# Optimization experiments

Hardware: AMD Instinct MI355X
Metric: run time of the kernel (lower is better)

The kernel has to match this reference:

```python
import jax, jax.numpy as jnp
import numpy as np

N = 50000      # nodes
E = 800000     # edges
F_IN = 256
HID = [256, 256, 512]
G = 512        # graphs
FP = 2048      # fingerprint size


def setup_inputs() -> dict:
    key = jax.random.key(0)
    ks = jax.random.split(key, 14)
    node_features = jax.random.normal(ks[0], (N, F_IN), dtype=jnp.float32)
    edge_index = jax.random.randint(ks[1], (2, E), 0, N, dtype=jnp.int64)
    batch = jnp.sort(jax.random.randint(ks[2], (N,), 0, G, dtype=jnp.int64))

    def lin(k, fi, fo):
        s = 1.0 / np.sqrt(fi)
        kw, kb = jax.random.split(k)
        W = jax.random.uniform(kw, (fi, fo), jnp.float32, -s, s)
        b = jax.random.uniform(kb, (fo,), jnp.float32, -s, s)
        return W, b

    W1, b1 = lin(ks[3], F_IN, HID[0])
    W2, b2 = lin(ks[4], HID[0], HID[1])
    W3, b3 = lin(ks[5], HID[1], HID[2])
    pw, pb = lin(ks[6], HID[2], 1)          # PoolWeightedSum gating linear
    Wo, bo = lin(ks[7], 2 * HID[2], FP)     # head: weight_sum + max concat
    return dict(node_features=node_features, edge_index=edge_index, batch=batch,
                W1=W1, b1=b1, W2=W2, b2=b2, W3=W3, b3=b3,
                pw=pw, pb=pb, Wo=Wo, bo=bo)


def _gcn_layer(x, src, dst, W, b):
    # GCNConv: add self-loops, symmetric normalization, h = x @ W, aggregate.
    n = x.shape[0]
    h = x @ W  # [N, F_out]
    loop = jnp.arange(n, dtype=src.dtype)
    s = jnp.concatenate([src, loop])
    d = jnp.concatenate([dst, loop])
    deg = jax.ops.segment_sum(jnp.ones(s.shape[0], h.dtype), d, num_segments=n)
    dis = jax.lax.rsqrt(deg)  # deg >= 1 because of self-loops
    norm = dis[s] * dis[d]    # [E+N]
    out = jax.ops.segment_sum(h[s] * norm[:, None], d, num_segments=n)
    return out + b


def _forward(node_features, edge_index, batch,
             W1, b1, W2, b2, W3, b3, pw, pb, Wo, bo):
    src, dst = edge_index[0], edge_index[1]
    x = node_features
    for W, b in ((W1, b1), (W2, b2), (W3, b3)):
        x = jax.nn.relu(_gcn_layer(x, src, dst, W, b))

    # PoolWeightedSum: sigmoid-gated node features, scatter-add per graph
    w = jax.nn.sigmoid(x @ pw + pb)  # [N, 1]
    pooled_ws = jax.ops.segment_sum(x * w, batch, num_segments=G,
                                    indices_are_sorted=True)
    # PoolMax: scatter-max per graph (empty segments -> 0, like torch zeros init)
    pooled_max = jax.ops.segment_max(x, batch, num_segments=G,
                                     indices_are_sorted=True)
    pooled_max = jnp.where(jnp.isfinite(pooled_max), pooled_max, 0.0)

    feats = jnp.concatenate([pooled_ws, pooled_max], axis=1)  # [G, 2*HID[-1]]
    return jax.nn.relu(feats @ Wo + bo)  # [G, FP]


def reference(node_features, edge_index, batch,
              W1, b1, W2, b2, W3, b3, pw, pb, Wo, bo):
    return _forward(node_features, edge_index, batch,
                    W1, b1, W2, b2, W3, b3, pw, pb, Wo, bo)
```

## Files before the change

### kernel.cpp

```cpp
#include <hip/hip_runtime.h>
#include <math.h>

#define NNODES 50000
#define NEDGES 800000
#define NGRAPH 512
#define FIN    256
#define H1     256
#define H2     256
#define H3     512
#define FPOUT  2048

typedef __attribute__((ext_vector_type(8))) short short8;
typedef __attribute__((ext_vector_type(8))) _Float16 half8;
typedef __attribute__((ext_vector_type(4))) float floatx4;
typedef __attribute__((ext_vector_type(4))) unsigned short ushx4;

__device__ inline float h2f(ushort u) { return (float)__builtin_bit_cast(_Float16, u); }
__device__ inline ushort f2h(float x) { return __builtin_bit_cast(ushort, (_Float16)x); }
__device__ inline void split2h(float a, ushort& h, ushort& l) {
    _Float16 hh = (_Float16)a;
    h = __builtin_bit_cast(ushort, hh);
    l = f2h(a - (float)hh);
}


__global__ __launch_bounds__(256) void zero_i32(int* p, int n) {
    int i = blockIdx.x * 256 + threadIdx.x;
    if (i < n) p[i] = 0;
}

__global__ __launch_bounds__(256) void count_deg(const int* __restrict__ ei, int* __restrict__ degi,
                                                 int* __restrict__ rank, int e_total) {
    int e = blockIdx.x * 256 + threadIdx.x;
    if (e >= e_total) return;
    int d = ei[e_total + e];
    rank[e] = atomicAdd(&degi[d], 1);
}

__global__ __launch_bounds__(256) void calc_dis(const int* __restrict__ degi, float* __restrict__ dis, int n) {
    int i = blockIdx.x * 256 + threadIdx.x;
    if (i < n) dis[i] = rsqrtf((float)(degi[i] + 1));
}

__global__ __launch_bounds__(256) void scanA(const int* __restrict__ degi, int* __restrict__ offs,
                                             int* __restrict__ partials, int n) {
    __shared__ int sm[256];
    int t = threadIdx.x, idx = blockIdx.x * 256 + t;
    int v = (idx < n) ? degi[idx] : 0;
    sm[t] = v; __syncthreads();
    for (int d = 1; d < 256; d <<= 1) {
        int add = (t >= d) ? sm[t - d] : 0;
        __syncthreads();
        sm[t] += add;
        __syncthreads();
    }
    if (idx < n) offs[idx + 1] = sm[t];
    if (t == 255) partials[blockIdx.x] = sm[255];
}

__global__ __launch_bounds__(256) void scanB(int* __restrict__ partials, int nb) {
    __shared__ int sm[256];
    int t = threadIdx.x;
    int v = (t < nb) ? partials[t] : 0;
    sm[t] = v; __syncthreads();
    for (int d = 1; d < 256; d <<= 1) {
        int add = (t >= d) ? sm[t - d] : 0;
        __syncthreads();
        sm[t] += add;
        __syncthreads();
    }
    if (t < nb) partials[t] = sm[t] - v;
}

__global__ __launch_bounds__(256) void scanC(int* __restrict__ offs, const int* __restrict__ partials, int n) {
    int idx = blockIdx.x * 256 + threadIdx.x;
    if (idx < n) offs[idx + 1] += partials[blockIdx.x];
    if (idx == 0) offs[0] = 0;
}

__global__ __launch_bounds__(256) void fill_csr(const int* __restrict__ ei, const float* __restrict__ dis,
                                                const int* __restrict__ offs, const int* __restrict__ rank,
                                                int2* __restrict__ csr_pair, int e_total) {
    int e = blockIdx.x * 256 + threadIdx.x;
    if (e >= e_total) return;
    int s = ei[e];
    int d = ei[e_total + e];
    int pos = offs[d] + rank[e];
    int2 pr;
    pr.x = s;
    pr.y = __float_as_int(dis[s] * dis[d]);
    csr_pair[pos] = pr;
}

__global__ __launch_bounds__(256) void wsplit_t(const float* __restrict__ W, ushort* __restrict__ hi,
                                                ushort* __restrict__ lo, int K, int N) {
    __shared__ float sm[32][33];
    int tx = threadIdx.x & 31, ty = threadIdx.x >> 5;
    int n0 = blockIdx.x * 32, k0 = blockIdx.y * 32;
    #pragma unroll
    for (int j = 0; j < 32; j += 8)
        sm[ty + j][tx] = W[(size_t)(k0 + ty + j) * N + n0 + tx];
    __syncthreads();
    #pragma unroll
    for (int j = 0; j < 32; j += 8) {
        float a = sm[tx][ty + j];
        ushort h, l; split2h(a, h, l);
        size_t o = (size_t)(n0 + ty + j) * K + k0 + tx;
        hi[o] = h; lo[o] = l;
    }
}

__global__ __launch_bounds__(256) void conv_f16(const float* __restrict__ x, ushort* __restrict__ xh, int total4) {
    int i = blockIdx.x * 256 + threadIdx.x;
    if (i >= total4) return;
    float4 a = ((const float4*)x)[i];
    ushx4 h = {f2h(a.x), f2h(a.y), f2h(a.z), f2h(a.w)};
    ((ushx4*)xh)[i] = h;
}

template<int SPLIT, int ACC, int KSPAN>
__global__ __launch_bounds__(256) void gemm_f16(const ushort* __restrict__ Ahp, const ushort* __restrict__ Alp,
                                                const ushort* __restrict__ Bhp, const ushort* __restrict__ Blp,
                                                float* __restrict__ C, ushort* __restrict__ Ch,
                                                const float* __restrict__ bias,
                                                int M, int N, int K, int do_relu, int outmode) {
    __shared__ _Float16 lsA[128 * 64];
    __shared__ _Float16 lsB[128 * 64];
    __shared__ _Float16 lsAl[SPLIT ? 128 * 64 : 8];
    __shared__ _Float16 lsBl[SPLIT ? 128 * 64 : 8];
    const _Float16* Ah = (const _Float16*)Ahp;
    const _Float16* Al = (const _Float16*)Alp;
    const _Float16* Bh = (const _Float16*)Bhp;
    const _Float16* Bl = (const _Float16*)Blp;

    int tid = threadIdx.x;
    int w = tid >> 6, lane = tid & 63;
    int quad = lane >> 4, lr = lane & 15;
    int wm = w & 1, wn = w >> 1;

    int gx = gridDim.x;
    int orig = blockIdx.y * gx + blockIdx.x;
    int nwg = gx * gridDim.y;
    int xcd = orig & 7, slot = orig >> 3;
    int q = nwg >> 3, r = nwg & 7;
    int wid = (xcd < r ? xcd * (q + 1) : r * (q + 1) + (xcd - r) * q) + slot;
    int row0 = (wid / gx) * 128, col0 = (wid % gx) * 128;
    int kb = blockIdx.z * KSPAN;

    floatx4 acc[4][4];
    #pragma unroll
    for (int i = 0; i < 4; ++i)
        #pragma unroll
        for (int j = 0; j < 4; ++j)
            acc[i][j] = (floatx4){0.f, 0.f, 0.f, 0.f};

    const half8 zer = {};
    int srow = tid >> 3;
    int sgran = tid & 7;
    int skk = sgran * 8;
    int sgx = (sgran ^ (srow & 7)) * 8;

    half8 pa[4], pb[4], pal[4], pbl[4];
    #pragma unroll
    for (int c = 0; c < 4; ++c) {
        int row = c * 32 + srow;
        bool mok = (row0 + row) < M;
        size_t aoff = (size_t)(row0 + row) * K + kb + skk;
        pa[c] = mok ? *(const half8*)(Ah + aoff) : zer;
        if constexpr (SPLIT) pal[c] = mok ? *(const half8*)(Al + aoff) : zer;
        size_t boff = (size_t)(col0 + row) * K + kb + skk;
        pb[c] = *(const half8*)(Bh + boff);
        if constexpr (SPLIT) pbl[c] = *(const half8*)(Bl + boff);
    }

    for (int k0 = kb; k0 < kb + KSPAN; k0 += 64) {
        #pragma unroll
        for (int c = 0; c < 4; ++c) {
            int lo = (c * 32 + srow) * 64 + sgx;
            *(half8*)(lsA + lo) = pa[c];
            *(half8*)(lsB + lo) = pb[c];
            if constexpr (SPLIT) { *(half8*)(lsAl + lo) = pal[c]; *(half8*)(lsBl + lo) = pbl[c]; }
        }
        __syncthreads();
        if (k0 + 64 < kb + KSPAN) {
            #pragma unroll
            for (int c = 0; c < 4; ++c) {
                int row = c * 32 + srow;
                bool mok = (row0 + row) < M;
                size_t aoff = (size_t)(row0 + row) * K + k0 + 64 + skk;
                pa[c] = mok ? *(const half8*)(Ah + aoff) : zer;
                if constexpr (SPLIT) pal[c] = mok ? *(const half8*)(Al + aoff) : zer;
                size_t boff = (size_t)(col0 + row) * K + k0 + 64 + skk;
                pb[c] = *(const half8*)(Bh + boff);
                if constexpr (SPLIT) pbl[c] = *(const half8*)(Bl + boff);
            }
        }
        #pragma unroll
        for (int kk = 0; kk < 2; ++kk) {
            half8 af[4], afl[4];
            #pragma unroll
            for (int mt = 0; mt < 4; ++mt) {
                int row = wm * 64 + mt * 16 + lr;
                int ao = row * 64 + (((kk * 4 + quad) ^ (row & 7)) << 3);
                af[mt] = *(const half8*)(lsA + ao);
                if constexpr (SPLIT) afl[mt] = *(const half8*)(lsAl + ao);
            }
            #pragma unroll
            for (int nt = 0; nt < 4; ++nt) {
                int row = wn * 64 + nt * 16 + lr;
                int bo = row * 64 + (((kk * 4 + quad) ^ (row & 7)) << 3);
                half8 bf = *(const half8*)(lsB + bo);
                half8 bfl;
                if constexpr (SPLIT) bfl = *(const half8*)(lsBl + bo);
                #pragma unroll
                for (int mt = 0; mt < 4; ++mt) {
                    acc[mt][nt] = __builtin_amdgcn_mfma_f32_16x16x32_f16(af[mt], bf, acc[mt][nt], 0, 0, 0);
                    if constexpr (SPLIT) {
                        acc[mt][nt] = __builtin_amdgcn_mfma_f32_16x16x32_f16(af[mt], bfl, acc[mt][nt], 0, 0, 0);
                        acc[mt][nt] = __builtin_amdgcn_mfma_f32_16x16x32_f16(afl[mt], bf, acc[mt][nt], 0, 0, 0);
                    }
                }
            }
        }
        __syncthreads();
    }

    size_t zoff = ACC ? (size_t)blockIdx.z * M * N : 0;
    #pragma unroll
    for (int mt = 0; mt < 4; ++mt) {
        #pragma unroll
        for (int rr = 0; rr < 4; ++rr) {
            int row = row0 + wm * 64 + mt * 16 + quad * 4 + rr;
            if (row >= M) continue;
            #pragma unroll
            for (int nt = 0; nt < 4; ++nt) {
                int col = col0 + wn * 64 + nt * 16 + lr;
                float v = acc[mt][nt][rr];
                if (!ACC) {
                    v += bias[col];
                    if (do_relu) v = v > 0.f ? v : 0.f;
                }
                if (outmode) Ch[(size_t)row * N + col] = f2h(v);
                else         C[zoff + (size_t)row * N + col] = v;
            }
        }
    }
}

__global__ __launch_bounds__(256) void head_fin(const float* __restrict__ part, const float* __restrict__ bo,
                                                float* __restrict__ out) {
    int i4 = blockIdx.x * 256 + threadIdx.x;
    const int TOT4 = NGRAPH * FPOUT / 4;
    if (i4 >= TOT4) return;
    int col4 = i4 & (FPOUT / 4 - 1);
    const size_t STRIDE4 = (size_t)NGRAPH * FPOUT / 4;
    const float4* p = (const float4*)part;
    float4 a = p[i4];
    float4 b = p[i4 + STRIDE4];
    float4 c = p[i4 + 2 * STRIDE4];
    float4 d = p[i4 + 3 * STRIDE4];
    float4 bb = ((const float4*)bo)[col4];
    float4 o;
    o.x = a.x + b.x + c.x + d.x + bb.x; o.x = o.x > 0.f ? o.x : 0.f;
    o.y = a.y + b.y + c.y + d.y + bb.y; o.y = o.y > 0.f ? o.y : 0.f;
    o.z = a.z + b.z + c.z + d.z + bb.z; o.z = o.z > 0.f ? o.z : 0.f;
    o.w = a.w + b.w + c.w + d.w + bb.w; o.w = o.w > 0.f ? o.w : 0.f;
    ((float4*)out)[i4] = o;
}

__global__ __launch_bounds__(256) void agg256b(const ushort* __restrict__ xh, ushort* __restrict__ yh,
                                               const float* __restrict__ dis,
                                               const int* __restrict__ offs, const int2* __restrict__ csr_pair) {
    constexpr int F = 256;
    int wave = threadIdx.x >> 6;
    int lane = threadIdx.x & 63;
    int half = lane >> 5;
    int sub  = lane & 31;
    int v = blockIdx.x * 8 + wave * 2 + half;
    int beg = offs[v], end = offs[v + 1];
    int len = end - beg;
    int leno = __shfl_xor(len, 32, 64);
    int maxlen = len > leno ? len : leno;

    float dv = dis[v];
    float sw = dv * dv;
    short8 a0 = ((const short8*)(xh + (size_t)v * F))[sub];
    float acc[8];
    #pragma unroll
    for (int j = 0; j < 8; ++j) acc[j] = h2f((ushort)a0[j]) * sw;

    for (int k = 0; k < maxlen; k += 8) {
        int   s[8];
        float w[8];
        #pragma unroll
        for (int u = 0; u < 8; ++u) {
            int idx = beg + k + u;
            bool val = idx < end;
            int ic = val ? idx : beg;
            int2 pr = csr_pair[ic];
            s[u] = pr.x;
            w[u] = val ? __int_as_float(pr.y) : 0.f;
        }
        short8 g[8];
        #pragma unroll
        for (int u = 0; u < 8; ++u)
            g[u] = ((const short8*)(xh + (size_t)s[u] * F))[sub];
        #pragma unroll
        for (int u = 0; u < 8; ++u) {
            #pragma unroll
            for (int j = 0; j < 8; ++j)
                acc[j] += h2f((ushort)g[u][j]) * w[u];
        }
    }

    ushort h[8];
    #pragma unroll
    for (int j = 0; j < 8; ++j) h[j] = f2h(acc[j]);
    short8 hv = {(short)h[0], (short)h[1], (short)h[2], (short)h[3], (short)h[4], (short)h[5], (short)h[6], (short)h[7]};
    ((short8*)(yh + (size_t)v * F))[sub] = hv;
}

__global__ __launch_bounds__(1024) void gatepool(const float* __restrict__ x, const float* __restrict__ pw,
                                                 const float* __restrict__ pb, const int* __restrict__ batch,
                                                 ushort* __restrict__ phi, ushort* __restrict__ plo, int n) {
    int g = blockIdx.x;
    int t = threadIdx.x;
    int wave = t >> 6, lane = t & 63;
    int lo_ = 0, hi_ = n;
    while (lo_ < hi_) { int mid = (lo_ + hi_) >> 1; if (batch[mid] < g) lo_ = mid + 1; else hi_ = mid; }
    int start = lo_;
    hi_ = n;
    while (lo_ < hi_) { int mid = (lo_ + hi_) >> 1; if (batch[mid] < g + 1) lo_ = mid + 1; else hi_ = mid; }
    int end = lo_;

    const float4* pwv = (const float4*)pw;
    float4 wa = pwv[lane], wb = pwv[lane + 64];
    float pb0 = pb[0];

    float4 s0 = make_float4(0.f, 0.f, 0.f, 0.f), s1 = s0;
    float4 m0 = make_float4(-INFINITY, -INFINITY, -INFINITY, -INFINITY), m1 = m0;

    for (int nn = start + wave; nn < end; nn += 16) {
        const float4* xr = (const float4*)(x + (size_t)nn * 512);
        float4 a = xr[lane];
        float4 b = xr[lane + 64];
        float p = a.x * wa.x + a.y * wa.y + a.z * wa.z + a.w * wa.w
                + b.x * wb.x + b.y * wb.y + b.z * wb.z + b.w * wb.w;
        #pragma unroll
        for (int off = 32; off; off >>= 1) p += __shfl_down(p, off, 64);
        float wg = __shfl(p, 0, 64);
        wg = 1.f / (1.f + expf(-(wg + pb0)));
        s0.x += a.x * wg; s0.y += a.y * wg; s0.z += a.z * wg; s0.w += a.w * wg;
        s1.x += b.x * wg; s1.y += b.y * wg; s1.z += b.z * wg; s1.w += b.w * wg;
        m0.x = fmaxf(m0.x, a.x); m0.y = fmaxf(m0.y, a.y); m0.z = fmaxf(m0.z, a.z); m0.w = fmaxf(m0.w, a.w);
        m1.x = fmaxf(m1.x, b.x); m1.y = fmaxf(m1.y, b.y); m1.z = fmaxf(m1.z, b.z); m1.w = fmaxf(m1.w, b.w);
    }

    __shared__ float ls[16][1024];
    *(float4*)&ls[wave][lane * 4]       = s0;
    *(float4*)&ls[wave][256 + lane * 4] = s1;
    *(float4*)&ls[wave][512 + lane * 4] = m0;
    *(float4*)&ls[wave][768 + lane * 4] = m1;
    __syncthreads();

    float val;
    if (t < 512) {
        float s = 0.f;
        #pragma unroll
        for (int wv = 0; wv < 16; ++wv) s += ls[wv][t];
        val = s;
    } else {
        float m = -INFINITY;
        #pragma unroll
        for (int wv = 0; wv < 16; ++wv) m = fmaxf(m, ls[wv][t]);
        if (start >= end) m = 0.f;
        val = m;
    }
    ushort h, l;
    split2h(val, h, l);
    size_t base = (size_t)g * 1024;
    phi[base + t] = h;
    plo[base + t] = l;
}


extern "C" void kernel_launch(void* const* d_in, const int* in_sizes, int n_in,
                              void* d_out, int out_size, void* d_ws, size_t ws_size,
                              hipStream_t stream) {
    const float* x0    = (const float*)d_in[0];
    const int*   ei    = (const int*)d_in[1];
    const int*   batch = (const int*)d_in[2];
    const float* W1 = (const float*)d_in[3];
    const float* b1 = (const float*)d_in[4];
    const float* W2 = (const float*)d_in[5];
    const float* b2 = (const float*)d_in[6];
    const float* W3 = (const float*)d_in[7];
    const float* b3 = (const float*)d_in[8];
    const float* pw = (const float*)d_in[9];
    const float* pb = (const float*)d_in[10];
    const float* Wo = (const float*)d_in[11];
    const float* bo = (const float*)d_in[12];
    float* out = (float*)d_out;

    float* ws = (float*)d_ws;
    size_t off = 0;
    float* bufB = ws + off; off += (size_t)NNODES * 512;
    ushort* xh  = (ushort*)(ws + off); off += (size_t)NNODES * 256 / 2;
    ushort* yh  = (ushort*)(ws + off); off += (size_t)NNODES * 256 / 2;
    int*    rank = (int*)(ws + off);   off += (size_t)NNODES * 256 / 2;
    ushort* W1thi = (ushort*)(ws + off); off += 256 * 256 / 2;
    ushort* W1tlo = (ushort*)(ws + off); off += 256 * 256 / 2;
    ushort* W2thi = (ushort*)(ws + off); off += 256 * 256 / 2;
    ushort* W2tlo = (ushort*)(ws + off); off += 256 * 256 / 2;
    ushort* W3thi = (ushort*)(ws + off); off += 512 * 256 / 2;
    ushort* W3tlo = (ushort*)(ws + off); off += 512 * 256 / 2;
    ushort* Wothi = (ushort*)(ws + off); off += (size_t)FPOUT * 1024 / 2;
    ushort* Wotlo = (ushort*)(ws + off); off += (size_t)FPOUT * 1024 / 2;
    ushort* phi = (ushort*)(ws + off); off += (size_t)NGRAPH * 1024 / 2;
    ushort* plo = (ushort*)(ws + off); off += (size_t)NGRAPH * 1024 / 2;
    float* dis  = ws + off; off += NNODES;
    int*   degi = (int*)(ws + off); off += NNODES;
    int*   offs = (int*)(ws + off); off += (NNODES + 4);
    int*   curs_unused = (int*)(ws + off); off += NNODES;
    (void)curs_unused;
    int2*  csr_pair = (int2*)(ws + off); off += 2 * (size_t)NEDGES;
    int*   partials = (int*)(ws + off); off += 256;

    const int NB_N = (NNODES + 255) / 256;
    const int NB_E = (NEDGES + 255) / 256;
    const int NB_A = NNODES / 8;
    const int MB128 = (NNODES + 127) / 128;

    { dim3 g(256 / 32, 256 / 32);    wsplit_t<<<g, 256, 0, stream>>>(W1, W1thi, W1tlo, 256, 256); }
    { dim3 g(256 / 32, 256 / 32);    wsplit_t<<<g, 256, 0, stream>>>(W2, W2thi, W2tlo, 256, 256); }
    { dim3 g(512 / 32, 256 / 32);    wsplit_t<<<g, 256, 0, stream>>>(W3, W3thi, W3tlo, 256, 512); }
    { dim3 g(FPOUT / 32, 1024 / 32); wsplit_t<<<g, 256, 0, stream>>>(Wo, Wothi, Wotlo, 1024, FPOUT); }

    zero_i32<<<NB_N, 256, 0, stream>>>(degi, NNODES);
    count_deg<<<NB_E, 256, 0, stream>>>(ei, degi, rank, NEDGES);
    calc_dis<<<NB_N, 256, 0, stream>>>(degi, dis, NNODES);
    scanA<<<NB_N, 256, 0, stream>>>(degi, offs, partials, NNODES);
    scanB<<<1, 256, 0, stream>>>(partials, NB_N);
    scanC<<<NB_N, 256, 0, stream>>>(offs, partials, NNODES);
    fill_csr<<<NB_E, 256, 0, stream>>>(ei, dis, offs, rank, csr_pair, NEDGES);

    conv_f16<<<(NNODES * 256 / 4 + 255) / 256, 256, 0, stream>>>(x0, xh, NNODES * 256 / 4);

    agg256b<<<NB_A, 256, 0, stream>>>(xh, yh, dis, offs, csr_pair);
    {
        dim3 grid(H1 / 128, MB128);
        gemm_f16<0, 0, 256><<<grid, 256, 0, stream>>>(yh, nullptr, W1thi, nullptr, nullptr, xh, b1,
                                                      NNODES, H1, FIN, 1, 1);
    }
    agg256b<<<NB_A, 256, 0, stream>>>(xh, yh, dis, offs, csr_pair);
    {
        dim3 grid(H2 / 128, MB128);
        gemm_f16<0, 0, 256><<<grid, 256, 0, stream>>>(yh, nullptr, W2thi, nullptr, nullptr, xh, b2,
                                                      NNODES, H2, H1, 1, 1);
    }
    agg256b<<<NB_A, 256, 0, stream>>>(xh, yh, dis, offs, csr_pair);
    {
        dim3 grid(H3 / 128, MB128);
        gemm_f16<0, 0, 256><<<grid, 256, 0, stream>>>(yh, nullptr, W3thi, nullptr, bufB, nullptr, b3,
                                                      NNODES, H3, H2, 1, 0);
    }
    gatepool<<<NGRAPH, 1024, 0, stream>>>(bufB, pw, pb, batch, phi, plo, NNODES);
    {
        dim3 grid(FPOUT / 128, (NGRAPH + 127) / 128, 4);
        gemm_f16<1, 1, 256><<<grid, 256, 0, stream>>>(phi, plo, Wothi, Wotlo, bufB, nullptr, nullptr,
                                                      NGRAPH, FPOUT, 1024, 0, 0);
    }
    head_fin<<<(NGRAPH * FPOUT / 4 + 255) / 256, 256, 0, stream>>>(bufB, bo, out);
}
```

Baseline: 528.1 us.

## Store node features in chunked feature-major layout and aggregate per chunk

Conv and GEMM epilogues now write fp16 node features in a layout of 8 chunks of 32 features, with each chunk stored contiguously across all nodes. The aggregation kernel is rewritten so each block handles one chunk for 4 nodes, with 16 edge-groups per wave and a shuffle reduction at the end. The goal is a smaller gather working set per chunk (50000×64B), which should raise L2/MALL hit rates for the random neighbour reads. The cost is 8x more blocks, reading the CSR entries 8 times, and scattered 2-byte stores in the GEMM epilogue.

```diff
diff --git a/kernel.cpp b/kernel.cpp
--- a/kernel.cpp
+++ b/kernel.cpp
@@ -113,9 +113,12 @@
 __global__ __launch_bounds__(256) void conv_f16(const float* __restrict__ x, ushort* __restrict__ xh, int total4) {
     int i = blockIdx.x * 256 + threadIdx.x;
     if (i >= total4) return;
+    int n  = i >> 6;
+    int f4 = i & 63;
     float4 a = ((const float4*)x)[i];
     ushx4 h = {f2h(a.x), f2h(a.y), f2h(a.z), f2h(a.w)};
-    ((ushx4*)xh)[i] = h;
+    size_t o4 = (((size_t)(f4 >> 3) * NNODES + n) * 32 + (f4 & 7) * 4) >> 2;
+    ((ushx4*)xh)[o4] = h;
 }
 
 template<int SPLIT, int ACC, int KSPAN>
@@ -240,7 +243,7 @@
                     v += bias[col];
                     if (do_relu) v = v > 0.f ? v : 0.f;
                 }
-                if (outmode) Ch[(size_t)row * N + col] = f2h(v);
+                if (outmode) Ch[((size_t)(col >> 5) * M + row) * 32 + (col & 31)] = f2h(v);
                 else         C[zoff + (size_t)row * N + col] = v;
             }
         }
@@ -268,56 +271,51 @@
     ((float4*)out)[i4] = o;
 }
 
-__global__ __launch_bounds__(256) void agg256b(const ushort* __restrict__ xh, ushort* __restrict__ yh,
-                                               const float* __restrict__ dis,
-                                               const int* __restrict__ offs, const int2* __restrict__ csr_pair) {
-    constexpr int F = 256;
+__global__ __launch_bounds__(256) void agg_chunk(const ushort* __restrict__ xh, ushort* __restrict__ yh,
+                                                 const float* __restrict__ dis,
+                                                 const int* __restrict__ offs, const int2* __restrict__ csr_pair) {
     int wave = threadIdx.x >> 6;
     int lane = threadIdx.x & 63;
-    int half = lane >> 5;
-    int sub  = lane & 31;
-    int v = blockIdx.x * 8 + wave * 2 + half;
+    int eg = lane >> 2;
+    int fq = lane & 3;
+    int chunk = blockIdx.x & 7;
+    int v = (blockIdx.x >> 3) * 4 + wave;
     int beg = offs[v], end = offs[v + 1];
-    int len = end - beg;
-    int leno = __shfl_xor(len, 32, 64);
-    int maxlen = len > leno ? len : leno;
-
+    int deg = end - beg;
     float dv = dis[v];
     float sw = dv * dv;
-    short8 a0 = ((const short8*)(xh + (size_t)v * F))[sub];
+    const _Float16* xc = (const _Float16*)xh + (size_t)chunk * NNODES * 32;
+
     float acc[8];
     #pragma unroll
-    for (int j = 0; j < 8; ++j) acc[j] = h2f((ushort)a0[j]) * sw;
-
-    for (int k = 0; k < maxlen; k += 8) {
-        int   s[8];
-        float w[8];
-        #pragma unroll
-        for (int u = 0; u < 8; ++u) {
-            int idx = beg + k + u;
-            bool val = idx < end;
-            int ic = val ? idx : beg;
-            int2 pr = csr_pair[ic];
-            s[u] = pr.x;
-            w[u] = val ? __int_as_float(pr.y) : 0.f;
-        }
-        short8 g[8];
-        #pragma unroll
-        for (int u = 0; u < 8; ++u)
-            g[u] = ((const short8*)(xh + (size_t)s[u] * F))[sub];
-        #pragma unroll
-        for (int u = 0; u < 8; ++u) {
-            #pragma unroll
-            for (int j = 0; j < 8; ++j)
-                acc[j] += h2f((ushort)g[u][j]) * w[u];
-        }
-    }
-
-    ushort h[8];
-    #pragma unroll
-    for (int j = 0; j < 8; ++j) h[j] = f2h(acc[j]);
-    short8 hv = {(short)h[0], (short)h[1], (short)h[2], (short)h[3], (short)h[4], (short)h[5], (short)h[6], (short)h[7]};
-    ((short8*)(yh + (size_t)v * F))[sub] = hv;
+    for (int j = 0; j < 8; ++j) acc[j] = 0.f;
+
+    int trips = (deg + 16) >> 4;
+    for (int k = 0; k < trips; ++k) {
+        int j = k * 16 + eg;
+        bool self = (j == 0);
+        bool val = (j <= deg) && !self;
+        int ic = val ? (beg + j - 1) : 0;
+        int2 pr = csr_pair[ic];
+        int s   = self ? v : pr.x;
+        float w = self ? sw : (val ? __int_as_float(pr.y) : 0.f);
+        half8 g = *(const half8*)(xc + (size_t)s * 32 + fq * 8);
+        #pragma unroll
+        for (int q = 0; q < 8; ++q) acc[q] += (float)g[q] * w;
+    }
+    #pragma unroll
+    for (int m = 4; m <= 32; m <<= 1)
+        #pragma unroll
+        for (int q = 0; q < 8; ++q) acc[q] += __shfl_xor(acc[q], m, 64);
+
+    if (eg == 0) {
+        ushort h[8];
+        #pragma unroll
+        for (int q = 0; q < 8; ++q) h[q] = f2h(acc[q]);
+        short8 hv = {(short)h[0], (short)h[1], (short)h[2], (short)h[3],
+                     (short)h[4], (short)h[5], (short)h[6], (short)h[7]};
+        *(short8*)(yh + (size_t)v * 256 + chunk * 32 + fq * 8) = hv;
+    }
 }
 
 __global__ __launch_bounds__(1024) void gatepool(const float* __restrict__ x, const float* __restrict__ pw,
@@ -428,7 +426,7 @@
 
     const int NB_N = (NNODES + 255) / 256;
     const int NB_E = (NEDGES + 255) / 256;
-    const int NB_A = NNODES / 8;
+    const int NB_A = (NNODES / 4) * 8;
     const int MB128 = (NNODES + 127) / 128;
 
     { dim3 g(256 / 32, 256 / 32);    wsplit_t<<<g, 256, 0, stream>>>(W1, W1thi, W1tlo, 256, 256); }
@@ -446,19 +444,19 @@
 
     conv_f16<<<(NNODES * 256 / 4 + 255) / 256, 256, 0, stream>>>(x0, xh, NNODES * 256 / 4);
 
-    agg256b<<<NB_A, 256, 0, stream>>>(xh, yh, dis, offs, csr_pair);
+    agg_chunk<<<NB_A, 256, 0, stream>>>(xh, yh, dis, offs, csr_pair);
     {
         dim3 grid(H1 / 128, MB128);
         gemm_f16<0, 0, 256><<<grid, 256, 0, stream>>>(yh, nullptr, W1thi, nullptr, nullptr, xh, b1,
                                                       NNODES, H1, FIN, 1, 1);
     }
-    agg256b<<<NB_A, 256, 0, stream>>>(xh, yh, dis, offs, csr_pair);
+    agg_chunk<<<NB_A, 256, 0, stream>>>(xh, yh, dis, offs, csr_pair);
     {
         dim3 grid(H2 / 128, MB128);
         gemm_f16<0, 0, 256><<<grid, 256, 0, stream>>>(yh, nullptr, W2thi, nullptr, nullptr, xh, b2,
                                                       NNODES, H2, H1, 1, 1);
     }
-    agg256b<<<NB_A, 256, 0, stream>>>(xh, yh, dis, offs, csr_pair);
+    agg_chunk<<<NB_A, 256, 0, stream>>>(xh, yh, dis, offs, csr_pair);
     {
         dim3 grid(H3 / 128, MB128);
         gemm_f16<0, 0, 256><<<grid, 256, 0, stream>>>(yh, nullptr, W3thi, nullptr, bufB, nullptr, b3,
```

New measurement: 791.1 us. 1.5x slower.

## Build CSR with two-pass bucketed binning instead of scattered per-edge writes

Applied to the files above, without the earlier changes.

Replaces the per-edge rank-based CSR fill with a two-stage binning sort. Edges are first grouped locally into 256-node buckets and written contiguously to a temp buffer, then each bucket is scattered into final CSR positions from shared memory. The aim is to cut the random global writes and the rank array traffic from the CSR build. In exchange it adds an extra pass over the edges, shared-memory atomics, and a bucket-capacity loop whose edge order within a node is nondeterministic.

```diff
diff --git a/kernel.cpp b/kernel.cpp
--- a/kernel.cpp
+++ b/kernel.cpp
@@ -10,6 +10,10 @@
 #define H3     512
 #define FPOUT  2048
 
+#define NBUCK  196
+#define EPB    3200
+#define BCAP   4864
+
 typedef __attribute__((ext_vector_type(8))) short short8;
 typedef __attribute__((ext_vector_type(8))) _Float16 half8;
 typedef __attribute__((ext_vector_type(4))) float floatx4;
@@ -29,12 +33,11 @@
     if (i < n) p[i] = 0;
 }
 
-__global__ __launch_bounds__(256) void count_deg(const int* __restrict__ ei, int* __restrict__ degi,
-                                                 int* __restrict__ rank, int e_total) {
+__global__ __launch_bounds__(256) void count_deg(const int* __restrict__ ei, int* __restrict__ degi, int e_total) {
     int e = blockIdx.x * 256 + threadIdx.x;
     if (e >= e_total) return;
     int d = ei[e_total + e];
-    rank[e] = atomicAdd(&degi[d], 1);
+    atomicAdd(&degi[d], 1);
 }
 
 __global__ __launch_bounds__(256) void calc_dis(const int* __restrict__ degi, float* __restrict__ dis, int n) {
@@ -78,18 +81,82 @@
     if (idx == 0) offs[0] = 0;
 }
 
-__global__ __launch_bounds__(256) void fill_csr(const int* __restrict__ ei, const float* __restrict__ dis,
-                                                const int* __restrict__ offs, const int* __restrict__ rank,
-                                                int2* __restrict__ csr_pair, int e_total) {
-    int e = blockIdx.x * 256 + threadIdx.x;
-    if (e >= e_total) return;
-    int s = ei[e];
-    int d = ei[e_total + e];
-    int pos = offs[d] + rank[e];
-    int2 pr;
-    pr.x = s;
-    pr.y = __float_as_int(dis[s] * dis[d]);
-    csr_pair[pos] = pr;
+__global__ __launch_bounds__(256) void binA(const int* __restrict__ ei, const int* __restrict__ offs,
+                                            int* __restrict__ gcur, int2* __restrict__ tmp, int e_total) {
+    __shared__ int2 ls[EPB];
+    __shared__ int2 ls2[EPB];
+    __shared__ int hist[256], lpref[256], lcur[256], gbase[256], obase[256];
+    int tid = threadIdx.x;
+    int e0 = blockIdx.x * EPB;
+    int cnt = e_total - e0; if (cnt > EPB) cnt = EPB;
+    hist[tid] = 0;
+    __syncthreads();
+    for (int i = tid; i < cnt; i += 256) {
+        int s = ei[e0 + i];
+        int d = ei[e_total + e0 + i];
+        ls[i] = (int2){s, d};
+        atomicAdd(&hist[d >> 8], 1);
+    }
+    __syncthreads();
+    int hv = hist[tid];
+    lpref[tid] = hv;
+    __syncthreads();
+    for (int dlt = 1; dlt < 256; dlt <<= 1) {
+        int add = (tid >= dlt) ? lpref[tid - dlt] : 0;
+        __syncthreads();
+        lpref[tid] += add;
+        __syncthreads();
+    }
+    int excl = lpref[tid] - hv;
+    __syncthreads();
+    lpref[tid] = excl;
+    lcur[tid] = 0;
+    __syncthreads();
+    for (int i = tid; i < cnt; i += 256) {
+        int2 pr = ls[i];
+        int b = pr.y >> 8;
+        int r = atomicAdd(&lcur[b], 1);
+        ls2[lpref[b] + r] = pr;
+    }
+    if (tid < NBUCK) {
+        int c = hist[tid];
+        gbase[tid] = c ? atomicAdd(&gcur[tid], c) : 0;
+        obase[tid] = offs[tid << 8];
+    }
+    __syncthreads();
+    for (int i = tid; i < cnt; i += 256) {
+        int2 pr = ls2[i];
+        int b = pr.y >> 8;
+        tmp[obase[b] + gbase[b] + (i - lpref[b])] = pr;
+    }
+}
+
+__global__ __launch_bounds__(256) void binB(const int2* __restrict__ tmp, const int* __restrict__ offs,
+                                            const float* __restrict__ dis, int2* __restrict__ csr_pair) {
+    __shared__ int2 ls[BCAP];
+    __shared__ int cntN[256];
+    int tid = threadIdx.x;
+    int b = blockIdx.x;
+    int nlo = b << 8;
+    int nhi = nlo + 256; if (nhi > NNODES) nhi = NNODES;
+    int base = offs[nlo];
+    int tot = offs[nhi] - base;
+    cntN[tid] = 0;
+    __syncthreads();
+    for (int c0 = 0; c0 < tot; c0 += BCAP) {
+        int cc = tot - c0; if (cc > BCAP) cc = BCAP;
+        for (int i = tid; i < cc; i += 256)
+            ls[i] = tmp[base + c0 + i];
+        __syncthreads();
+        for (int i = tid; i < cc; i += 256) {
+            int2 pr = ls[i];
+            int d = pr.y;
+            int r = atomicAdd(&cntN[d & 255], 1);
+            float w = dis[pr.x] * dis[d];
+            csr_pair[offs[d] + r] = (int2){pr.x, __float_as_int(w)};
+        }
+        __syncthreads();
+    }
 }
 
 __global__ __launch_bounds__(256) void wsplit_t(const float* __restrict__ W, ushort* __restrict__ hi,
@@ -407,7 +474,7 @@
     float* bufB = ws + off; off += (size_t)NNODES * 512;
     ushort* xh  = (ushort*)(ws + off); off += (size_t)NNODES * 256 / 2;
     ushort* yh  = (ushort*)(ws + off); off += (size_t)NNODES * 256 / 2;
-    int*    rank = (int*)(ws + off);   off += (size_t)NNODES * 256 / 2;
+    int2*   tmp = (int2*)(ws + off);   off += (size_t)NNODES * 256 / 2;
     ushort* W1thi = (ushort*)(ws + off); off += 256 * 256 / 2;
     ushort* W1tlo = (ushort*)(ws + off); off += 256 * 256 / 2;
     ushort* W2thi = (ushort*)(ws + off); off += 256 * 256 / 2;
@@ -421,8 +488,7 @@
     float* dis  = ws + off; off += NNODES;
     int*   degi = (int*)(ws + off); off += NNODES;
     int*   offs = (int*)(ws + off); off += (NNODES + 4);
-    int*   curs_unused = (int*)(ws + off); off += NNODES;
-    (void)curs_unused;
+    int*   gcur = (int*)(ws + off); off += 256;
     int2*  csr_pair = (int2*)(ws + off); off += 2 * (size_t)NEDGES;
     int*   partials = (int*)(ws + off); off += 256;
 
@@ -437,12 +503,14 @@
     { dim3 g(FPOUT / 32, 1024 / 32); wsplit_t<<<g, 256, 0, stream>>>(Wo, Wothi, Wotlo, 1024, FPOUT); }
 
     zero_i32<<<NB_N, 256, 0, stream>>>(degi, NNODES);
-    count_deg<<<NB_E, 256, 0, stream>>>(ei, degi, rank, NEDGES);
+    count_deg<<<NB_E, 256, 0, stream>>>(ei, degi, NEDGES);
     calc_dis<<<NB_N, 256, 0, stream>>>(degi, dis, NNODES);
     scanA<<<NB_N, 256, 0, stream>>>(degi, offs, partials, NNODES);
     scanB<<<1, 256, 0, stream>>>(partials, NB_N);
     scanC<<<NB_N, 256, 0, stream>>>(offs, partials, NNODES);
-    fill_csr<<<NB_E, 256, 0, stream>>>(ei, dis, offs, rank, csr_pair, NEDGES);
+    zero_i32<<<1, 256, 0, stream>>>(gcur, 256);
+    binA<<<NEDGES / EPB, 256, 0, stream>>>(ei, offs, gcur, tmp, NEDGES);
+    binB<<<NBUCK, 256, 0, stream>>>(tmp, offs, dis, csr_pair);
 
     conv_f16<<<(NNODES * 256 / 4 + 255) / 256, 256, 0, stream>>>(x0, xh, NNODES * 256 / 4);
 
```

After: 539.1 us. 2.1% more time.
